# Optimization experiments

Hardware: AMD Instinct MI355X
Metric: run time of the kernel (lower is better)

## Reference

```python
import jax, jax.numpy as jnp
import numpy as np

N_SAMPLES_DEPTHS = [64, 32, 16]
DEPTH_RES_LEVELS = [2, 2, 2]
NV = 3
IMG_H = IMG_W = 512
VOL = 128


def trilinear_lookup(vol, pts):
    """Trilinear sample of vol[D,H,W] at pts[...,3] in [-1,1] (x->W, y->H, z->D).
    Matches F.grid_sample(mode='bilinear', padding_mode='border', align_corners=True)."""
    D, H, W = vol.shape
    x = jnp.clip((pts[..., 0] + 1.0) * 0.5 * (W - 1), 0.0, W - 1.0)
    y = jnp.clip((pts[..., 1] + 1.0) * 0.5 * (H - 1), 0.0, H - 1.0)
    z = jnp.clip((pts[..., 2] + 1.0) * 0.5 * (D - 1), 0.0, D - 1.0)
    x0f = jnp.floor(x); y0f = jnp.floor(y); z0f = jnp.floor(z)
    wx = x - x0f; wy = y - y0f; wz = z - z0f
    x0 = x0f.astype(jnp.int32); y0 = y0f.astype(jnp.int32); z0 = z0f.astype(jnp.int32)
    x1 = jnp.minimum(x0 + 1, W - 1)
    y1 = jnp.minimum(y0 + 1, H - 1)
    z1 = jnp.minimum(z0 + 1, D - 1)
    c000 = vol[z0, y0, x0]; c001 = vol[z0, y0, x1]
    c010 = vol[z0, y1, x0]; c011 = vol[z0, y1, x1]
    c100 = vol[z1, y0, x0]; c101 = vol[z1, y0, x1]
    c110 = vol[z1, y1, x0]; c111 = vol[z1, y1, x1]
    c00 = c000 * (1 - wx) + c001 * wx
    c01 = c010 * (1 - wx) + c011 * wx
    c10 = c100 * (1 - wx) + c101 * wx
    c11 = c110 * (1 - wx) + c111 * wx
    c0 = c00 * (1 - wy) + c01 * wy
    c1 = c10 * (1 - wy) + c11 * wy
    return c0 * (1 - wz) + c1 * wz


def _make_c2w(angle):
    c, s = np.cos(angle), np.sin(angle)
    m = np.eye(4, dtype=np.float32)
    m[:3, :3] = np.array([[c, 0, s], [0, 1, 0], [-s, 0, c]], np.float32)
    m[:3, 3] = np.array([0.3 * np.sin(angle), 0.0, -1.5], np.float32)
    return m


def setup_inputs() -> dict:
    key = jax.random.key(0)
    k_img, k_vol = jax.random.split(key)
    imgs = jax.random.normal(k_img, (NV, 3, IMG_H, IMG_W), dtype=jnp.float32)
    f = 400.0
    intr = np.array([[f, 0.0, IMG_W / 2], [0.0, f, IMG_H / 2], [0.0, 0.0, 1.0]], np.float32)
    intrs = jnp.asarray(np.stack([intr] * NV))
    c2ws = jnp.asarray(np.stack([_make_c2w(a) for a in (0.0, 0.15, -0.15)]))
    near_fars = jnp.tile(jnp.array([[0.5, 3.0]], jnp.float32), (NV, 1))
    density_volume = jax.random.normal(k_vol, (VOL, VOL, VOL), dtype=jnp.float32)
    return {"imgs": imgs, "intrs": intrs, "c2ws": c2ws, "near_fars": near_fars,
            "density_volume": density_volume, "stage_idx": 0}


def reference(imgs, intrs, c2ws, near_fars, density_volume, stage_idx):
    img_h, img_w = imgs.shape[-2:]
    res = DEPTH_RES_LEVELS[stage_idx]
    h, w = img_h // res, img_w // res
    n_s = N_SAMPLES_DEPTHS[stage_idx]

    # pixel grid at reduced resolution (matches torch.meshgrid 'ij')
    ty = jnp.linspace(0.0, img_h - 1.0, h)
    tx = jnp.linspace(0.0, img_w - 1.0, w)
    py, px = jnp.meshgrid(ty, tx, indexing='ij')
    pixels = jnp.stack([px.reshape(-1), py.reshape(-1), jnp.ones(h * w, jnp.float32)], -1)  # [N,3]
    t_lin = jnp.linspace(0.0, 1.0, n_s)  # [S]

    def render_view(c2w, intr, near_far):
        cam = pixels @ jnp.linalg.inv(intr).T                      # [N,3]
        rays_d = cam / jnp.linalg.norm(cam, axis=-1, keepdims=True)
        rays_d = rays_d @ c2w[:3, :3].T                            # world-space dirs
        z_vals = near_far[0] + (near_far[1] - near_far[0]) * t_lin  # [S] (single stage: already sorted)
        pts = c2w[None, None, :3, 3] + rays_d[:, None, :] * z_vals[None, :, None]  # [N,S,3]
        outside = jax.lax.stop_gradient((jnp.linalg.norm(pts, axis=-1) > 1.0).astype(pts.dtype))  # [N,S]
        density = trilinear_lookup(density_volume, pts)            # [N,S]
        weights = jax.nn.softmax(density, axis=-1)
        cam_rays_d = rays_d @ jnp.linalg.inv(c2w[:3, :3]).T        # back to camera frame
        render_z = jnp.sum(z_vals[None, :] * weights, axis=1)      # [N]
        render_depth = (render_z * cam_rays_d[:, 2]).reshape(h, w)
        occ_reg = density[:, :6].mean() + (density * outside).sum() / (outside.sum() + 1e-10)
        depth_full = jax.image.resize(render_depth, (img_h, img_w), method='bilinear')
        return depth_full, occ_reg

    depths, occs = jax.vmap(render_view)(c2ws, intrs, near_fars)
    # views other than src_idx=0 are rendered under no_grad in the original
    depths = jnp.concatenate([depths[:1], jax.lax.stop_gradient(depths[1:])], axis=0)
    occs = jnp.concatenate([occs[:1], jax.lax.stop_gradient(occs[1:])], axis=0)
    return depths, occs
```

## Files before the change

kernel.cpp:

```cpp
#include <hip/hip_runtime.h>
#include <hip/hip_fp16.h>
#include <math.h>

#define NVIEW 3
#define HLOW 256
#define WLOW 256
#define NPIX (HLOW * WLOW)
#define NS 64
#define VOLN 128
#define IMGH 512
#define IMGW 512
#define BLK 256
#define BLOCKS_PER_VIEW (NPIX / BLK)
#define NVOX (VOLN * VOLN * VOLN)
#define UPS2_BLOCKS ((NVIEW * IMGH * IMGW / 2) / BLK)
#define NXCD 8
#define MARCH_BLOCKS (NVIEW * BLOCKS_PER_VIEW)
#define CHUNK (MARCH_BLOCKS / NXCD)

struct Ray {
    float ax0, axs, ay0, ays, az0, azs;
    float sLo, sHi;
    float z0, zstep, ncz;
};

__device__ __forceinline__ Ray ray_setup(
    int view, int row, int col,
    const float* __restrict__ intrs, const float* __restrict__ c2ws,
    const float* __restrict__ nf)
{
    const float px = 511.0f * (float)col * (1.0f / 255.0f);
    const float py = 511.0f * (float)row * (1.0f / 255.0f);

    const float* K = intrs + view * 9;
    const float a = K[0], b = K[1], c = K[2];
    const float d = K[3], e = K[4], f = K[5];
    const float g = K[6], h = K[7], i9 = K[8];
    const float det = a * (e * i9 - f * h) - b * (d * i9 - f * g) + c * (d * h - e * g);
    const float id = 1.0f / det;
    const float m00 = (e * i9 - f * h) * id, m01 = -(b * i9 - c * h) * id, m02 = (b * f - c * e) * id;
    const float m10 = -(d * i9 - f * g) * id, m11 = (a * i9 - c * g) * id, m12 = -(a * f - c * d) * id;
    const float m20 = (d * h - e * g) * id, m21 = -(a * h - b * g) * id, m22 = (a * e - b * d) * id;

    const float cx = m00 * px + m01 * py + m02;
    const float cy = m10 * px + m11 * py + m12;
    const float cz = m20 * px + m21 * py + m22;
    const float inr = rsqrtf(cx * cx + cy * cy + cz * cz);
    const float ncx = cx * inr, ncy = cy * inr, ncz = cz * inr;

    const float* M = c2ws + view * 16;
    const float dx = M[0] * ncx + M[1] * ncy + M[2] * ncz;
    const float dy = M[4] * ncx + M[5] * ncy + M[6] * ncz;
    const float dz = M[8] * ncx + M[9] * ncy + M[10] * ncz;
    const float tx = M[3], ty = M[7], tz = M[11];

    const float z0 = nf[view * 2 + 0];
    const float zstep = (nf[view * 2 + 1] - z0) * (1.0f / 63.0f);

    Ray r;
    const float gx0 = (tx + 1.0f) * 63.5f, gxs = dx * 63.5f;
    const float gy0 = (ty + 1.0f) * 63.5f, gys = dy * 63.5f;
    const float gz0 = (tz + 1.0f) * 63.5f, gzs = dz * 63.5f;
    r.ax0 = fmaf(gxs, z0, gx0); r.axs = gxs * zstep;
    r.ay0 = fmaf(gys, z0, gy0); r.ays = gys * zstep;
    r.az0 = fmaf(gzs, z0, gz0); r.azs = gzs * zstep;

    const float bq = tx * dx + ty * dy + tz * dz;
    const float cq = tx * tx + ty * ty + tz * tz;
    const float disc = bq * bq - (cq - 1.0f);
    if (disc >= 0.0f) {
        const float rt = sqrtf(disc);
        const float inv = 1.0f / zstep;
        r.sLo = (-bq - rt - z0) * inv;
        r.sHi = (-bq + rt - z0) * inv;
    } else {
        r.sLo = 3.4e38f;
        r.sHi = 0.0f;
    }

    r.z0 = z0;
    r.zstep = zstep;
    r.ncz = ncz;
    return r;
}

__global__ __launch_bounds__(BLK) void build_quad_kernel(
    const float* __restrict__ vol, uint4* __restrict__ F)
{
    const int id = blockIdx.x * BLK + threadIdx.x;
    const int x = id & 127;
    const int y = (id >> 7) & 127;
    const int z = id >> 14;
    const int yp = min(y + 1, 127);
    const int zp = min(z + 1, 127);
    const int xb = min(x, 126);
    const int sel = x - xb;

    const float2 v00 = *reinterpret_cast<const float2*>(vol + (z  * VOLN + y ) * VOLN + xb);
    const float2 v01 = *reinterpret_cast<const float2*>(vol + (z  * VOLN + yp) * VOLN + xb);
    const float2 v10 = *reinterpret_cast<const float2*>(vol + (zp * VOLN + y ) * VOLN + xb);
    const float2 v11 = *reinterpret_cast<const float2*>(vol + (zp * VOLN + yp) * VOLN + xb);

    const float c000 = sel ? v00.y : v00.x, c001 = v00.y;
    const float c010 = sel ? v01.y : v01.x, c011 = v01.y;
    const float c100 = sel ? v10.y : v10.x, c101 = v10.y;
    const float c110 = sel ? v11.y : v11.x, c111 = v11.y;

    const __half2 w0 = __floats2half2_rn(c000, c100);
    const __half2 w1 = __floats2half2_rn(c001, c101);
    const __half2 w2 = __floats2half2_rn(c010, c110);
    const __half2 w3 = __floats2half2_rn(c011, c111);
    uint4 o;
    o.x = *reinterpret_cast<const unsigned*>(&w0);
    o.y = *reinterpret_cast<const unsigned*>(&w1);
    o.z = *reinterpret_cast<const unsigned*>(&w2);
    o.w = *reinterpret_cast<const unsigned*>(&w3);
    F[id] = o;
}

__global__ __launch_bounds__(BLK) void raymarch_quad_kernel(
    const float* __restrict__ intrs, const float* __restrict__ c2ws,
    const float* __restrict__ nf, const uint4* __restrict__ F,
    float* __restrict__ depth_low, float* __restrict__ partials)
{
    const int wg  = blockIdx.x;
    const int swz = (wg & (NXCD - 1)) * CHUNK + (wg >> 3);
    const int view = swz >> 8;
    const int row  = swz & 255;
    const int t    = threadIdx.x;

    const Ray r = ray_setup(view, row, t, intrs, c2ws, nf);

    float lsum = 0.0f, sacc = 0.0f;
    float d6 = 0.0f, dout = 0.0f, cnt = 0.0f;

    for (int sb = 0; sb < NS; sb += 8) {
        unsigned offs[8];
        float fxs[8], fys[8], fzs[8];

        #pragma unroll
        for (int i = 0; i < 8; ++i) {
            const float sf = (float)(sb + i);
            float gx = fmaf(r.axs, sf, r.ax0);
            float gy = fmaf(r.ays, sf, r.ay0);
            float gz = fmaf(r.azs, sf, r.az0);
            gx = fminf(fmaxf(gx, 0.0f), 127.0f);
            gy = fminf(fmaxf(gy, 0.0f), 127.0f);
            gz = fminf(fmaxf(gz, 0.0f), 127.0f);
            const float xbf = fminf(floorf(gx), 126.0f);
            const float ybf = fminf(floorf(gy), 126.0f);
            const float zbf = fminf(floorf(gz), 126.0f);
            fxs[i] = gx - xbf;
            fys[i] = gy - ybf;
            fzs[i] = gz - zbf;
            offs[i] = (unsigned)fmaf(zbf, 16384.0f, fmaf(ybf, 128.0f, xbf));
        }

        uint4 q[8];
        #pragma unroll
        for (int i = 0; i < 8; ++i) q[i] = F[offs[i]];

        #pragma unroll
        for (int i = 0; i < 8; ++i) {
            const float sf = (float)(sb + i);
            union { unsigned u; __half2 h; } a0, a1, b0, b1;
            a0.u = q[i].x; a1.u = q[i].y; b0.u = q[i].z; b1.u = q[i].w;

            const __half2 fxh = __float2half2_rn(fxs[i]);
            const __half2 fyh = __float2half2_rn(fys[i]);
            const __half2 cx0 = __hfma2(fxh, __hsub2(a1.h, a0.h), a0.h);
            const __half2 cx1 = __hfma2(fxh, __hsub2(b1.h, b0.h), b0.h);
            const __half2 cy  = __hfma2(fyh, __hsub2(cx1, cx0), cx0);
            const float c0 = __low2float(cy);
            const float c1 = __high2float(cy);
            const float dens = fmaf(fzs[i], c1 - c0, c0);

            const float w = __expf(dens);
            lsum += w;
            sacc = fmaf(sf, w, sacc);

            if (sb == 0 && i < 6) d6 += dens;
            const bool o = (sf < r.sLo) || (sf > r.sHi);
            dout += o ? dens : 0.0f;
            cnt  += o ? 1.0f : 0.0f;
        }
    }

    depth_low[view * NPIX + row * WLOW + t] =
        fmaf(r.zstep, sacc / lsum, r.z0) * r.ncz;

    __shared__ float s0[BLK], s1[BLK], s2[BLK];
    s0[t] = d6; s1[t] = dout; s2[t] = cnt;
    __syncthreads();
    for (int off = BLK / 2; off > 0; off >>= 1) {
        if (t < off) {
            s0[t] += s0[t + off];
            s1[t] += s1[t + off];
            s2[t] += s2[t + off];
        }
        __syncthreads();
    }
    if (t == 0) {
        partials[swz * 3 + 0] = s0[0];
        partials[swz * 3 + 1] = s1[0];
        partials[swz * 3 + 2] = s2[0];
    }
}

__global__ __launch_bounds__(BLK) void raymarch_f32_kernel(
    const float* __restrict__ intrs, const float* __restrict__ c2ws,
    const float* __restrict__ nf, const float* __restrict__ vol,
    float* __restrict__ depth_low, float* __restrict__ partials)
{
    const int view = blockIdx.x >> 8;
    const int row  = blockIdx.x & 255;
    const int t    = threadIdx.x;

    const Ray r = ray_setup(view, row, t, intrs, c2ws, nf);

    float lsum = 0.0f, sacc = 0.0f;
    float d6 = 0.0f, dout = 0.0f, cnt = 0.0f;

    #pragma unroll 16
    for (int s = 0; s < NS; ++s) {
        const float sf = (float)s;
        float gx = fmaf(r.axs, sf, r.ax0);
        float gy = fmaf(r.ays, sf, r.ay0);
        float gz = fmaf(r.azs, sf, r.az0);
        gx = fminf(fmaxf(gx, 0.0f), 127.0f);
        gy = fminf(fmaxf(gy, 0.0f), 127.0f);
        gz = fminf(fmaxf(gz, 0.0f), 127.0f);
        const float xbf = fminf(floorf(gx), 126.0f);
        const float ybf = fminf(floorf(gy), 126.0f);
        const float zbf = fminf(floorf(gz), 126.0f);
        const float fx = gx - xbf, fy = gy - ybf, fz = gz - zbf;
        const unsigned off = (unsigned)fmaf(zbf, 16384.0f, fmaf(ybf, 128.0f, xbf));

        const float* p0 = vol + off;
        const float2 v00 = *reinterpret_cast<const float2*>(p0);
        const float2 v01 = *reinterpret_cast<const float2*>(p0 + VOLN);
        const float2 v10 = *reinterpret_cast<const float2*>(p0 + VOLN * VOLN);
        const float2 v11 = *reinterpret_cast<const float2*>(p0 + VOLN * VOLN + VOLN);

        const float c00 = fmaf(fx, v00.y - v00.x, v00.x);
        const float c01 = fmaf(fx, v01.y - v01.x, v01.x);
        const float c10 = fmaf(fx, v10.y - v10.x, v10.x);
        const float c11 = fmaf(fx, v11.y - v11.x, v11.x);
        const float c0 = fmaf(fy, c01 - c00, c00);
        const float c1 = fmaf(fy, c11 - c10, c10);
        const float dens = fmaf(fz, c1 - c0, c0);

        const float w = __expf(dens);
        lsum += w;
        sacc = fmaf(sf, w, sacc);

        if (s < 6) d6 += dens;
        const bool o = (sf < r.sLo) || (sf > r.sHi);
        dout += o ? dens : 0.0f;
        cnt  += o ? 1.0f : 0.0f;
    }

    depth_low[view * NPIX + row * WLOW + t] =
        fmaf(r.zstep, sacc / lsum, r.z0) * r.ncz;

    __shared__ float s0[BLK], s1[BLK], s2[BLK];
    s0[t] = d6; s1[t] = dout; s2[t] = cnt;
    __syncthreads();
    for (int off = BLK / 2; off > 0; off >>= 1) {
        if (t < off) {
            s0[t] += s0[t + off];
            s1[t] += s1[t + off];
            s2[t] += s2[t + off];
        }
        __syncthreads();
    }
    if (t == 0) {
        partials[blockIdx.x * 3 + 0] = s0[0];
        partials[blockIdx.x * 3 + 1] = s1[0];
        partials[blockIdx.x * 3 + 2] = s2[0];
    }
}

__global__ __launch_bounds__(BLK) void epilogue_kernel(
    const float* __restrict__ low, const float* __restrict__ partials,
    float* __restrict__ out)
{
    if (blockIdx.x >= UPS2_BLOCKS) {
        const int view = blockIdx.x - UPS2_BLOCKS;
        const int t = threadIdx.x;
        __shared__ float s0[BLK], s1[BLK], s2[BLK];
        const int bi = view * BLOCKS_PER_VIEW + t;
        s0[t] = partials[bi * 3 + 0];
        s1[t] = partials[bi * 3 + 1];
        s2[t] = partials[bi * 3 + 2];
        __syncthreads();
        for (int off = BLK / 2; off > 0; off >>= 1) {
            if (t < off) {
                s0[t] += s0[t + off];
                s1[t] += s1[t + off];
                s2[t] += s2[t + off];
            }
            __syncthreads();
        }
        if (t == 0) {
            out[NVIEW * IMGH * IMGW + view] =
                s0[0] * (1.0f / (float)(NPIX * 6)) + s1[0] / (s2[0] + 1e-10f);
        }
        return;
    }

    const int idx2 = blockIdx.x * BLK + threadIdx.x;
    const int view = idx2 / (IMGH * IMGW / 2);
    const int rem  = idx2 - view * (IMGH * IMGW / 2);
    const int rr = rem >> 8;
    const int cp = rem & 255;
    const int cc0 = cp * 2;

    const float sy = (float)rr * 0.5f - 0.25f;
    const float y0f = floorf(sy);
    const float wy = sy - y0f;
    const int y0 = (int)y0f;
    const int y0c = max(y0, 0), y1c = min(y0 + 1, HLOW - 1);
    const float* src = low + view * NPIX;
    const float* r0 = src + y0c * WLOW;
    const float* r1 = src + y1c * WLOW;

    float2 res;
    {
        const float sx = (float)cc0 * 0.5f - 0.25f;
        const float x0f = floorf(sx);
        const float wx = sx - x0f;
        const int x0 = (int)x0f;
        const int x0c = max(x0, 0), x1c = min(x0 + 1, WLOW - 1);
        const float top = r0[x0c] * (1.0f - wx) + r0[x1c] * wx;
        const float bot = r1[x0c] * (1.0f - wx) + r1[x1c] * wx;
        res.x = top * (1.0f - wy) + bot * wy;
    }
    {
        const int cc1 = cc0 + 1;
        const float sx = (float)cc1 * 0.5f - 0.25f;
        const float x0f = floorf(sx);
        const float wx = sx - x0f;
        const int x0 = (int)x0f;
        const int x0c = max(x0, 0), x1c = min(x0 + 1, WLOW - 1);
        const float top = r0[x0c] * (1.0f - wx) + r0[x1c] * wx;
        const float bot = r1[x0c] * (1.0f - wx) + r1[x1c] * wx;
        res.y = top * (1.0f - wy) + bot * wy;
    }
    *reinterpret_cast<float2*>(out + view * (IMGH * IMGW) + rr * IMGW + cc0) = res;
}

extern "C" void kernel_launch(void* const* d_in, const int* in_sizes, int n_in,
                              void* d_out, int out_size, void* d_ws, size_t ws_size,
                              hipStream_t stream) {
    const float* intrs = (const float*)d_in[1];
    const float* c2ws  = (const float*)d_in[2];
    const float* nf    = (const float*)d_in[3];
    const float* vol   = (const float*)d_in[4];
    float* out = (float*)d_out;

    const size_t quad_bytes  = (size_t)NVOX * 16;
    const size_t depth_bytes = (size_t)NVIEW * NPIX * 4;
    const size_t part_bytes  = (size_t)NVIEW * BLOCKS_PER_VIEW * 3 * 4;
    char* ws = (char*)d_ws;

    float* depth_low;
    float* partials;

    if (ws_size >= quad_bytes + depth_bytes + part_bytes) {
        uint4* F = (uint4*)ws;
        depth_low = (float*)(ws + quad_bytes);
        partials  = depth_low + NVIEW * NPIX;
        build_quad_kernel<<<NVOX / BLK, BLK, 0, stream>>>(vol, F);
        raymarch_quad_kernel<<<MARCH_BLOCKS, BLK, 0, stream>>>(
            intrs, c2ws, nf, F, depth_low, partials);
    } else {
        depth_low = (float*)ws;
        partials  = depth_low + NVIEW * NPIX;
        raymarch_f32_kernel<<<MARCH_BLOCKS, BLK, 0, stream>>>(
            intrs, c2ws, nf, vol, depth_low, partials);
    }

    epilogue_kernel<<<UPS2_BLOCKS + NVIEW, BLK, 0, stream>>>(depth_low, partials, out);
}
```

Measured before the change: 42.22 us.

## Double-buffer voxel gathers, prescale volume by log2e, use exp2, closed-form outside count

The quad raymarch kernel now issues the gathers for the next 8-sample batch before consuming the current one, using two register buffers, so memory latency can overlap with interpolation math. The packed half volume is prescaled by log2(e), so the kernel can call exp2f directly, and the density partial sums are rescaled on output. The per-sample outside count becomes a closed-form interval computation, and the clamp is changed to 126.9995 to drop the floor clamps. The prescaling adds half-precision rounding error and the clamp slightly changes edge interpolation. Double buffering raises register pressure and may cut occupancy.

```diff
diff --git a/kernel.cpp b/kernel.cpp
--- a/kernel.cpp
+++ b/kernel.cpp
@@ -18,6 +18,9 @@
 #define MARCH_BLOCKS (NVIEW * BLOCKS_PER_VIEW)
 #define CHUNK (MARCH_BLOCKS / NXCD)
 
+#define LOG2E     1.4426950408889634f
+#define INV_LOG2E 0.6931471805599453f
+
 struct Ray {
     float ax0, axs, ay0, ays, az0, azs;
     float sLo, sHi;
@@ -46,8 +49,9 @@
     const float cy = m10 * px + m11 * py + m12;
     const float cz = m20 * px + m21 * py + m22;
     const float inr = rsqrtf(cx * cx + cy * cy + cz * cz);
-    const float ncx = cx * inr, ncy = cy * inr, ncz = cz * inr;
-
+    const float ncz = cz * inr;
+
+    const float ncx = cx * inr, ncy = cy * inr;
     const float* M = c2ws + view * 16;
     const float dx = M[0] * ncx + M[1] * ncy + M[2] * ncz;
     const float dy = M[4] * ncx + M[5] * ncy + M[6] * ncz;
@@ -106,10 +110,10 @@
     const float c100 = sel ? v10.y : v10.x, c101 = v10.y;
     const float c110 = sel ? v11.y : v11.x, c111 = v11.y;
 
-    const __half2 w0 = __floats2half2_rn(c000, c100);
-    const __half2 w1 = __floats2half2_rn(c001, c101);
-    const __half2 w2 = __floats2half2_rn(c010, c110);
-    const __half2 w3 = __floats2half2_rn(c011, c111);
+    const __half2 w0 = __floats2half2_rn(c000 * LOG2E, c100 * LOG2E);
+    const __half2 w1 = __floats2half2_rn(c001 * LOG2E, c101 * LOG2E);
+    const __half2 w2 = __floats2half2_rn(c010 * LOG2E, c110 * LOG2E);
+    const __half2 w3 = __floats2half2_rn(c011 * LOG2E, c111 * LOG2E);
     uint4 o;
     o.x = *reinterpret_cast<const unsigned*>(&w0);
     o.y = *reinterpret_cast<const unsigned*>(&w1);
@@ -131,60 +135,74 @@
 
     const Ray r = ray_setup(view, row, t, intrs, c2ws, nf);
 
-    float lsum = 0.0f, sacc = 0.0f;
-    float d6 = 0.0f, dout = 0.0f, cnt = 0.0f;
-
-    for (int sb = 0; sb < NS; sb += 8) {
-        unsigned offs[8];
-        float fxs[8], fys[8], fzs[8];
-
-        #pragma unroll
-        for (int i = 0; i < 8; ++i) {
-            const float sf = (float)(sb + i);
-            float gx = fmaf(r.axs, sf, r.ax0);
-            float gy = fmaf(r.ays, sf, r.ay0);
-            float gz = fmaf(r.azs, sf, r.az0);
-            gx = fminf(fmaxf(gx, 0.0f), 127.0f);
-            gy = fminf(fmaxf(gy, 0.0f), 127.0f);
-            gz = fminf(fmaxf(gz, 0.0f), 127.0f);
-            const float xbf = fminf(floorf(gx), 126.0f);
-            const float ybf = fminf(floorf(gy), 126.0f);
-            const float zbf = fminf(floorf(gz), 126.0f);
-            fxs[i] = gx - xbf;
-            fys[i] = gy - ybf;
-            fzs[i] = gz - zbf;
-            offs[i] = (unsigned)fmaf(zbf, 16384.0f, fmaf(ybf, 128.0f, xbf));
+    const float ilo = ceilf(fmaxf(r.sLo, 0.0f));
+    const float ihi = floorf(fminf(r.sHi, 63.0f));
+    const float cnt = 64.0f - fmaxf(0.0f, ihi - ilo + 1.0f);
+
+    float lsum = 0.0f, sacc = 0.0f, d6 = 0.0f, dout = 0.0f;
+
+    float fxs[2][8], fys[2][8], fzs[2][8];
+    uint4 q[2][8];
+
+#define ADDR_BATCH(BK, SB)                                                    \
+    {                                                                         \
+        unsigned offs[8];                                                     \
+        _Pragma("unroll")                                                     \
+        for (int i = 0; i < 8; ++i) {                                         \
+            const float sf = (float)((SB) + i);                               \
+            float gx = fmaf(r.axs, sf, r.ax0);                                \
+            float gy = fmaf(r.ays, sf, r.ay0);                                \
+            float gz = fmaf(r.azs, sf, r.az0);                                \
+            gx = fminf(fmaxf(gx, 0.0f), 126.9995f);                           \
+            gy = fminf(fmaxf(gy, 0.0f), 126.9995f);                           \
+            gz = fminf(fmaxf(gz, 0.0f), 126.9995f);                           \
+            const float xbf = floorf(gx);                                     \
+            const float ybf = floorf(gy);                                     \
+            const float zbf = floorf(gz);                                     \
+            fxs[BK][i] = gx - xbf;                                            \
+            fys[BK][i] = gy - ybf;                                            \
+            fzs[BK][i] = gz - zbf;                                            \
+            offs[i] = (unsigned)fmaf(zbf, 16384.0f, fmaf(ybf, 128.0f, xbf));  \
+        }                                                                     \
+        _Pragma("unroll")                                                     \
+        for (int i = 0; i < 8; ++i) q[BK][i] = F[offs[i]];                    \
+    }
+
+#define CONSUME_BATCH(BK, SB)                                                 \
+    _Pragma("unroll")                                                         \
+    for (int i = 0; i < 8; ++i) {                                             \
+        const float sf = (float)((SB) + i);                                   \
+        union { unsigned u; __half2 h; } a0, a1, b0, b1;                      \
+        a0.u = q[BK][i].x; a1.u = q[BK][i].y;                                 \
+        b0.u = q[BK][i].z; b1.u = q[BK][i].w;                                 \
+        const __half2 fxh = __float2half2_rn(fxs[BK][i]);                     \
+        const __half2 fyh = __float2half2_rn(fys[BK][i]);                     \
+        const __half2 cx0 = __hfma2(fxh, __hsub2(a1.h, a0.h), a0.h);          \
+        const __half2 cx1 = __hfma2(fxh, __hsub2(b1.h, b0.h), b0.h);          \
+        const __half2 cy  = __hfma2(fyh, __hsub2(cx1, cx0), cx0);             \
+        const float c0 = __low2float(cy);                                     \
+        const float c1 = __high2float(cy);                                    \
+        const float dens = fmaf(fzs[BK][i], c1 - c0, c0);    \
+        const float w = exp2f(dens);                             \
+        lsum += w;                                                            \
+        sacc = fmaf(sf, w, sacc);                                             \
+        if ((SB) == 0 && i < 6) d6 += dens;                                   \
+        const bool o = (sf < r.sLo) || (sf > r.sHi);                          \
+        dout += o ? dens : 0.0f;                                              \
+    }
+
+    ADDR_BATCH(0, 0)
+    #pragma unroll
+    for (int b = 0; b < 8; ++b) {
+        if (b < 7) {
+            if (b & 1) { ADDR_BATCH(0, (b + 1) * 8) }
+            else       { ADDR_BATCH(1, (b + 1) * 8) }
         }
-
-        uint4 q[8];
-        #pragma unroll
-        for (int i = 0; i < 8; ++i) q[i] = F[offs[i]];
-
-        #pragma unroll
-        for (int i = 0; i < 8; ++i) {
-            const float sf = (float)(sb + i);
-            union { unsigned u; __half2 h; } a0, a1, b0, b1;
-            a0.u = q[i].x; a1.u = q[i].y; b0.u = q[i].z; b1.u = q[i].w;
-
-            const __half2 fxh = __float2half2_rn(fxs[i]);
-            const __half2 fyh = __float2half2_rn(fys[i]);
-            const __half2 cx0 = __hfma2(fxh, __hsub2(a1.h, a0.h), a0.h);
-            const __half2 cx1 = __hfma2(fxh, __hsub2(b1.h, b0.h), b0.h);
-            const __half2 cy  = __hfma2(fyh, __hsub2(cx1, cx0), cx0);
-            const float c0 = __low2float(cy);
-            const float c1 = __high2float(cy);
-            const float dens = fmaf(fzs[i], c1 - c0, c0);
-
-            const float w = __expf(dens);
-            lsum += w;
-            sacc = fmaf(sf, w, sacc);
-
-            if (sb == 0 && i < 6) d6 += dens;
-            const bool o = (sf < r.sLo) || (sf > r.sHi);
-            dout += o ? dens : 0.0f;
-            cnt  += o ? 1.0f : 0.0f;
-        }
-    }
+        if (b & 1) { CONSUME_BATCH(1, b * 8) }
+        else       { CONSUME_BATCH(0, b * 8) }
+    }
+#undef ADDR_BATCH
+#undef CONSUME_BATCH
 
     depth_low[view * NPIX + row * WLOW + t] =
         fmaf(r.zstep, sacc / lsum, r.z0) * r.ncz;
@@ -201,8 +219,8 @@
         __syncthreads();
     }
     if (t == 0) {
-        partials[swz * 3 + 0] = s0[0];
-        partials[swz * 3 + 1] = s1[0];
+        partials[swz * 3 + 0] = s0[0] * INV_LOG2E;
+        partials[swz * 3 + 1] = s1[0] * INV_LOG2E;
         partials[swz * 3 + 2] = s2[0];
     }
 }
@@ -218,8 +236,11 @@
 
     const Ray r = ray_setup(view, row, t, intrs, c2ws, nf);
 
-    float lsum = 0.0f, sacc = 0.0f;
-    float d6 = 0.0f, dout = 0.0f, cnt = 0.0f;
+    const float ilo = ceilf(fmaxf(r.sLo, 0.0f));
+    const float ihi = floorf(fminf(r.sHi, 63.0f));
+    const float cnt = 64.0f - fmaxf(0.0f, ihi - ilo + 1.0f);
+
+    float lsum = 0.0f, sacc = 0.0f, d6 = 0.0f, dout = 0.0f;
 
     #pragma unroll 16
     for (int s = 0; s < NS; ++s) {
@@ -227,12 +248,12 @@
         float gx = fmaf(r.axs, sf, r.ax0);
         float gy = fmaf(r.ays, sf, r.ay0);
         float gz = fmaf(r.azs, sf, r.az0);
-        gx = fminf(fmaxf(gx, 0.0f), 127.0f);
-        gy = fminf(fmaxf(gy, 0.0f), 127.0f);
-        gz = fminf(fmaxf(gz, 0.0f), 127.0f);
-        const float xbf = fminf(floorf(gx), 126.0f);
-        const float ybf = fminf(floorf(gy), 126.0f);
-        const float zbf = fminf(floorf(gz), 126.0f);
+        gx = fminf(fmaxf(gx, 0.0f), 126.9995f);
+        gy = fminf(fmaxf(gy, 0.0f), 126.9995f);
+        gz = fminf(fmaxf(gz, 0.0f), 126.9995f);
+        const float xbf = floorf(gx);
+        const float ybf = floorf(gy);
+        const float zbf = floorf(gz);
         const float fx = gx - xbf, fy = gy - ybf, fz = gz - zbf;
         const unsigned off = (unsigned)fmaf(zbf, 16384.0f, fmaf(ybf, 128.0f, xbf));
 
@@ -257,7 +278,6 @@
         if (s < 6) d6 += dens;
         const bool o = (sf < r.sLo) || (sf > r.sHi);
         dout += o ? dens : 0.0f;
-        cnt  += o ? 1.0f : 0.0f;
     }
 
     depth_low[view * NPIX + row * WLOW + t] =
```

After: 37.44 us. 1.13x faster.
